# Optimization experiments

Hardware: AMD Instinct MI355X
Metric: run time of the kernel (lower is better)

The kernel has to match this reference:

```python
import jax, jax.numpy as jnp
import numpy as np

NUM_HEADS = 8
D_MODEL = 512
D_Q = D_MODEL // NUM_HEADS
B, S = 4, 2048


def setup_inputs() -> dict:
    key = jax.random.key(0)
    ks = jax.random.split(key, 7)
    bound = 1.0 / np.sqrt(D_MODEL)  # kaiming_uniform with a=sqrt(5) on fan_in=d_model
    return {
        "x_query": jax.random.normal(ks[0], (B, S, D_MODEL), dtype=jnp.float32),
        "x_key": jax.random.normal(ks[1], (B, S, D_MODEL), dtype=jnp.float32),
        "x_value": jax.random.normal(ks[2], (B, S, D_MODEL), dtype=jnp.float32),
        "Q": jax.random.uniform(ks[3], (NUM_HEADS, D_MODEL, D_Q), minval=-bound, maxval=bound, dtype=jnp.float32),
        "K": jax.random.uniform(ks[4], (NUM_HEADS, D_MODEL, D_Q), minval=-bound, maxval=bound, dtype=jnp.float32),
        "V": jax.random.uniform(ks[5], (NUM_HEADS, D_MODEL, D_Q), minval=-bound, maxval=bound, dtype=jnp.float32),
        "Wout": jax.random.uniform(ks[6], (D_MODEL, D_MODEL), minval=-bound, maxval=bound, dtype=jnp.float32),
    }


def reference(x_query, x_key, x_value, Q, K, V, Wout):
    # per-head projections: [B,S,d_model] x [H,d_model,d_q] -> [B,H,S,d_q]
    q = jnp.einsum('bsd,hdq->bhsq', x_query, Q)
    k = jnp.einsum('bsd,hdq->bhsq', x_key, K)
    v = jnp.einsum('bsd,hdq->bhsq', x_value, V)
    scale = 1.0 / jnp.sqrt(jnp.asarray(q.shape[-1], q.dtype))
    scores = jnp.einsum('bhsq,bhtq->bhst', q, k) * scale  # [B,H,S,S]
    attn = jax.nn.softmax(scores, axis=-1)
    heads = jnp.einsum('bhst,bhtq->bhsq', attn, v)  # [B,H,S,d_q]
    # faithful to original: .view(B, S, -1) on [B,H,S,d_q] layout (no transpose)
    concat = heads.reshape(heads.shape[0], heads.shape[2], -1)
    return concat @ Wout.T
```

## Files before the change

kernel.cpp:

```cpp
#include <hip/hip_runtime.h>
#include <math.h>

#define BATCH 4
#define SEQ   2048
#define DM    512
#define NH    8
#define DQ    64
#define BS    (BATCH*SEQ)
#define BPAD  72
#define APAD  72

#define QSCALE 0.18033688011112042f

typedef short  short8  __attribute__((ext_vector_type(8)));
typedef float  floatx4 __attribute__((ext_vector_type(4)));
typedef unsigned short ushort8 __attribute__((ext_vector_type(8)));

__device__ __forceinline__ unsigned short f2bf(float f) {
    return (unsigned short)((__float_as_uint(f) + 0x8000u) >> 16);
}
__device__ __forceinline__ unsigned pack2bf(float a, float b) {
    unsigned ua = __float_as_uint(a) + 0x8000u;
    unsigned ub = __float_as_uint(b) + 0x8000u;
    return __builtin_amdgcn_perm(ub, ua, 0x07060302u);
}

__global__ __launch_bounds__(256) void convert_w_kernel(
    const float* __restrict__ Wq, const float* __restrict__ Wk,
    const float* __restrict__ Wv, const float* __restrict__ Wo,
    unsigned short* __restrict__ wt, unsigned short* __restrict__ wo)
{
    const int which = blockIdx.y;
    const int idx = blockIdx.x * 256 + threadIdx.x;
    if (which == 3) {
        float4 v = *(const float4*)(Wo + (size_t)idx * 4);
        uint2 o;
        o.x = pack2bf(v.x, v.y);
        o.y = pack2bf(v.z, v.w);
        *(uint2*)(wo + (size_t)idx * 4) = o;
    } else {
        const float* W = (which == 0) ? Wq : (which == 1) ? Wk : Wv;
        const int n   = idx >> 7;
        const int dd0 = (idx & 127) * 4;
        const int h = n >> 6, d = n & 63;
        uint2 o;
        o.x = pack2bf(W[((size_t)h * DM + dd0 + 0) * DQ + d],
                      W[((size_t)h * DM + dd0 + 1) * DQ + d]);
        o.y = pack2bf(W[((size_t)h * DM + dd0 + 2) * DQ + d],
                      W[((size_t)h * DM + dd0 + 3) * DQ + d]);
        *(uint2*)(wt + (size_t)which * (DM * DM) + (size_t)n * DM + dd0) = o;
    }
}

__global__ __launch_bounds__(256) void qkv_gemm_kernel(
    const float* __restrict__ Xq, const float* __restrict__ Xk,
    const float* __restrict__ Xv, const unsigned short* __restrict__ wt,
    unsigned short* __restrict__ Oq, unsigned short* __restrict__ Ok,
    unsigned short* __restrict__ Ovt)
{
    __shared__ unsigned short As[128][APAD];
    __shared__ unsigned short Bs[128][APAD];

    const int which = blockIdx.z;
    const float* X = (which == 0) ? Xq : (which == 1) ? Xk : Xv;
    const unsigned short* Bt = wt + (size_t)which * (DM * DM);

    const int m0 = blockIdx.x * 128;
    const int n0 = blockIdx.y * 128;
    const int t = threadIdx.x, w = t >> 6, lane = t & 63;
    const int quad = lane >> 4, qr = lane & 15;
    const int arow = t >> 4;
    const int acol = (t & 15) * 4;
    const int brow = t >> 3;
    const int bcol = (t & 7) * 8;
    const int mw = 64 * (w >> 1), nw = 64 * (w & 1);

    floatx4 acc[4][4] = {};
    float4  areg[8];
    ushort8 breg[4];

    #pragma unroll
    for (int i = 0; i < 8; ++i)
        areg[i] = *(const float4*)(X + (size_t)(m0 + i * 16 + arow) * DM + acol);
    #pragma unroll
    for (int i = 0; i < 4; ++i)
        breg[i] = *(const ushort8*)(Bt + (size_t)(n0 + i * 32 + brow) * DM + bcol);

    for (int k0 = 0; k0 < DM; k0 += 64) {
        __syncthreads();
        #pragma unroll
        for (int i = 0; i < 8; ++i) {
            uint2 o;
            o.x = pack2bf(areg[i].x, areg[i].y);
            o.y = pack2bf(areg[i].z, areg[i].w);
            *(uint2*)&As[i * 16 + arow][acol] = o;
        }
        #pragma unroll
        for (int i = 0; i < 4; ++i)
            *(ushort8*)&Bs[i * 32 + brow][bcol] = breg[i];
        __syncthreads();

        if (k0 + 64 < DM) {
            #pragma unroll
            for (int i = 0; i < 8; ++i)
                areg[i] = *(const float4*)(X + (size_t)(m0 + i * 16 + arow) * DM + k0 + 64 + acol);
            #pragma unroll
            for (int i = 0; i < 4; ++i)
                breg[i] = *(const ushort8*)(Bt + (size_t)(n0 + i * 32 + brow) * DM + k0 + 64 + bcol);
        }

        #pragma unroll
        for (int kh = 0; kh < 2; ++kh) {
            short8 af[4], bf[4];
            #pragma unroll
            for (int si = 0; si < 4; ++si)
                af[si] = *(const short8*)&As[mw + 16 * si + qr][kh * 32 + quad * 8];
            #pragma unroll
            for (int sj = 0; sj < 4; ++sj)
                bf[sj] = *(const short8*)&Bs[nw + 16 * sj + qr][kh * 32 + quad * 8];
            #pragma unroll
            for (int si = 0; si < 4; ++si)
                #pragma unroll
                for (int sj = 0; sj < 4; ++sj)
                    acc[si][sj] = __builtin_amdgcn_mfma_f32_16x16x32_bf16(
                        af[si], bf[sj], acc[si][sj], 0, 0, 0);
        }
    }

    const float osc = (which == 0) ? QSCALE : 1.0f;
    if (which < 2) {
        unsigned short* O = (which == 0) ? Oq : Ok;
        #pragma unroll
        for (int si = 0; si < 4; ++si) {
            #pragma unroll
            for (int sj = 0; sj < 4; ++sj) {
                const int col = n0 + nw + 16 * sj + qr;
                const int h = col >> 6, d = col & 63;
                #pragma unroll
                for (int r = 0; r < 4; ++r) {
                    const int row = m0 + mw + 16 * si + quad * 4 + r;
                    const int b = row >> 11, s = row & (SEQ - 1);
                    O[((size_t)(b * NH + h) * SEQ + s) * DQ + d] = f2bf(acc[si][sj][r] * osc);
                }
            }
        }
    } else {
        #pragma unroll
        for (int si = 0; si < 4; ++si) {
            #pragma unroll
            for (int sj = 0; sj < 4; ++sj) {
                const int col = n0 + nw + 16 * sj + qr;
                const int h = col >> 6, d = col & 63;
                #pragma unroll
                for (int r = 0; r < 4; ++r) {
                    const int row = m0 + mw + 16 * si + quad * 4 + r;
                    const int b = row >> 11, s = row & (SEQ - 1);
                    Ovt[((size_t)(b * NH + h) * DQ + d) * SEQ + s] = f2bf(acc[si][sj][r]);
                }
            }
        }
    }
}

__global__ __launch_bounds__(256) void out_gemm_kernel(
    const unsigned short* __restrict__ A, const unsigned short* __restrict__ Bt,
    float* __restrict__ C)
{
    __shared__ unsigned short As[64][APAD];
    __shared__ unsigned short Bs[128][APAD];

    const int m0 = blockIdx.x * 64;
    const int n0 = blockIdx.y * 128;
    const int t = threadIdx.x, w = t >> 6, lane = t & 63;
    const int quad = lane >> 4, qr = lane & 15;
    const int brow = t >> 3;
    const int bcol = (t & 7) * 8;
    const int mw = 32 * (w >> 1), nw = 64 * (w & 1);

    floatx4 acc[2][4] = {};
    ushort8 areg[2], breg[4];

    #pragma unroll
    for (int i = 0; i < 2; ++i)
        areg[i] = *(const ushort8*)(A + (size_t)(m0 + i * 32 + brow) * DM + bcol);
    #pragma unroll
    for (int i = 0; i < 4; ++i)
        breg[i] = *(const ushort8*)(Bt + (size_t)(n0 + i * 32 + brow) * DM + bcol);

    for (int k0 = 0; k0 < DM; k0 += 64) {
        __syncthreads();
        #pragma unroll
        for (int i = 0; i < 2; ++i)
            *(ushort8*)&As[i * 32 + brow][bcol] = areg[i];
        #pragma unroll
        for (int i = 0; i < 4; ++i)
            *(ushort8*)&Bs[i * 32 + brow][bcol] = breg[i];
        __syncthreads();

        if (k0 + 64 < DM) {
            #pragma unroll
            for (int i = 0; i < 2; ++i)
                areg[i] = *(const ushort8*)(A + (size_t)(m0 + i * 32 + brow) * DM + k0 + 64 + bcol);
            #pragma unroll
            for (int i = 0; i < 4; ++i)
                breg[i] = *(const ushort8*)(Bt + (size_t)(n0 + i * 32 + brow) * DM + k0 + 64 + bcol);
        }

        #pragma unroll
        for (int kh = 0; kh < 2; ++kh) {
            short8 af[2], bf[4];
            #pragma unroll
            for (int si = 0; si < 2; ++si)
                af[si] = *(const short8*)&As[mw + 16 * si + qr][kh * 32 + quad * 8];
            #pragma unroll
            for (int sj = 0; sj < 4; ++sj)
                bf[sj] = *(const short8*)&Bs[nw + 16 * sj + qr][kh * 32 + quad * 8];
            #pragma unroll
            for (int si = 0; si < 2; ++si)
                #pragma unroll
                for (int sj = 0; sj < 4; ++sj)
                    acc[si][sj] = __builtin_amdgcn_mfma_f32_16x16x32_bf16(
                        af[si], bf[sj], acc[si][sj], 0, 0, 0);
        }
    }

    #pragma unroll
    for (int si = 0; si < 2; ++si) {
        #pragma unroll
        for (int sj = 0; sj < 4; ++sj) {
            const int col = n0 + nw + 16 * sj + qr;
            #pragma unroll
            for (int r = 0; r < 4; ++r) {
                const int row = m0 + mw + 16 * si + quad * 4 + r;
                C[(size_t)row * DM + col] = acc[si][sj][r];
            }
        }
    }
}

__global__ __launch_bounds__(256) void attn_kernel(
    const unsigned short* __restrict__ Qp, const unsigned short* __restrict__ Kp,
    const unsigned short* __restrict__ Vtp, unsigned short* __restrict__ Hd)
{
    __shared__ unsigned short Qs[64][BPAD];
    __shared__ unsigned short Ks[64][BPAD];
    __shared__ unsigned short Vts[64][BPAD];
    __shared__ unsigned short Ps[64][BPAD];

    const int s0 = blockIdx.x * 64;
    const int h  = blockIdx.y;
    const int b  = blockIdx.z;
    const size_t bh    = (size_t)(b * NH + h);
    const size_t base  = bh * SEQ * DQ;
    const size_t vbase = bh * DQ * SEQ;

    const int t    = threadIdx.x;
    const int w    = t >> 6;
    const int lane = t & 63;
    const int quad = lane >> 4;
    const int qr   = lane & 15;

    {
        const unsigned short* g = Qp + base + (size_t)s0 * DQ;
        #pragma unroll
        for (int i = 0; i < 2; ++i) {
            const int c = t + 256 * i;
            const int row = c >> 3, col8 = (c & 7) * 8;
            *(ushort8*)&Qs[row][col8] = *(const ushort8*)(g + row * DQ + col8);
        }
    }
    __syncthreads();
    const short8 aq0 = *(const short8*)&Qs[16 * w + qr][quad * 8];
    const short8 aq1 = *(const short8*)&Qs[16 * w + qr][quad * 8 + 32];

    floatx4 acc_o[4] = {};
    float l_lane = 0.f;

    ushort8 kreg[2], vreg[2];
    {
        const unsigned short* gk = Kp + base;
        const unsigned short* gv = Vtp + vbase;
        #pragma unroll
        for (int i = 0; i < 2; ++i) {
            const int c = t + 256 * i;
            const int row = c >> 3, col8 = (c & 7) * 8;
            kreg[i] = *(const ushort8*)(gk + row * DQ + col8);
            vreg[i] = *(const ushort8*)(gv + (size_t)row * SEQ + col8);
        }
    }

    for (int kt = 0; kt < SEQ; kt += 64) {
        __syncthreads();
        #pragma unroll
        for (int i = 0; i < 2; ++i) {
            const int c = t + 256 * i;
            const int row = c >> 3, col8 = (c & 7) * 8;
            *(ushort8*)&Ks[row][col8]  = kreg[i];
            *(ushort8*)&Vts[row][col8] = vreg[i];
        }
        __syncthreads();

        if (kt + 64 < SEQ) {
            const unsigned short* gk = Kp + base + (size_t)(kt + 64) * DQ;
            const unsigned short* gv = Vtp + vbase + (kt + 64);
            #pragma unroll
            for (int i = 0; i < 2; ++i) {
                const int c = t + 256 * i;
                const int row = c >> 3, col8 = (c & 7) * 8;
                kreg[i] = *(const ushort8*)(gk + row * DQ + col8);
                vreg[i] = *(const ushort8*)(gv + (size_t)row * SEQ + col8);
            }
        }

        #pragma unroll
        for (int si = 0; si < 4; ++si) {
            const short8 ak0 = *(const short8*)&Ks[16 * si + qr][quad * 8];
            const short8 ak1 = *(const short8*)&Ks[16 * si + qr][quad * 8 + 32];
            floatx4 z = {0.f, 0.f, 0.f, 0.f};
            z = __builtin_amdgcn_mfma_f32_16x16x32_bf16(ak0, aq0, z, 0, 0, 0);
            z = __builtin_amdgcn_mfma_f32_16x16x32_bf16(ak1, aq1, z, 0, 0, 0);
            const float p0 = __builtin_amdgcn_exp2f(z[0]);
            const float p1 = __builtin_amdgcn_exp2f(z[1]);
            const float p2 = __builtin_amdgcn_exp2f(z[2]);
            const float p3 = __builtin_amdgcn_exp2f(z[3]);
            l_lane += (p0 + p1) + (p2 + p3);
            uint2 pk;
            pk.x = pack2bf(p0, p1);
            pk.y = pack2bf(p2, p3);
            *(uint2*)&Ps[16 * w + qr][16 * si + quad * 4] = pk;
        }

        const short8 ap0 = *(const short8*)&Ps[16 * w + qr][quad * 8];
        const short8 ap1 = *(const short8*)&Ps[16 * w + qr][quad * 8 + 32];
        #pragma unroll
        for (int c = 0; c < 4; ++c) {
            const short8 bv0 = *(const short8*)&Vts[16 * c + qr][quad * 8];
            const short8 bv1 = *(const short8*)&Vts[16 * c + qr][quad * 8 + 32];
            acc_o[c] = __builtin_amdgcn_mfma_f32_16x16x32_bf16(ap0, bv0, acc_o[c], 0, 0, 0);
            acc_o[c] = __builtin_amdgcn_mfma_f32_16x16x32_bf16(ap1, bv1, acc_o[c], 0, 0, 0);
        }
    }

    l_lane += __shfl_xor(l_lane, 16);
    l_lane += __shfl_xor(l_lane, 32);
    float inv_l[4];
    #pragma unroll
    for (int r = 0; r < 4; ++r)
        inv_l[r] = 1.0f / __shfl(l_lane, quad * 4 + r);

    #pragma unroll
    for (int c = 0; c < 4; ++c)
        #pragma unroll
        for (int r = 0; r < 4; ++r)
            Hd[base + (size_t)(s0 + 16 * w + quad * 4 + r) * DQ + 16 * c + qr] =
                f2bf(acc_o[c][r] * inv_l[r]);
}

extern "C" void kernel_launch(void* const* d_in, const int* in_sizes, int n_in,
                              void* d_out, int out_size, void* d_ws, size_t ws_size,
                              hipStream_t stream) {
    const float* xq = (const float*)d_in[0];
    const float* xk = (const float*)d_in[1];
    const float* xv = (const float*)d_in[2];
    const float* Qw = (const float*)d_in[3];
    const float* Kw = (const float*)d_in[4];
    const float* Vw = (const float*)d_in[5];
    const float* Wo = (const float*)d_in[6];
    float* out = (float*)d_out;

    unsigned short* ws = (unsigned short*)d_ws;
    unsigned short* wt    = ws;
    unsigned short* wo    = ws + (size_t)786432;
    unsigned short* q_ws  = ws + (size_t)1048576;
    unsigned short* k_ws  = ws + (size_t)5242880;
    unsigned short* vt_ws = ws + (size_t)9437184;
    unsigned short* h_ws  = ws + (size_t)13631488;

    convert_w_kernel<<<dim3(256, 4), 256, 0, stream>>>(Qw, Kw, Vw, Wo, wt, wo);
    qkv_gemm_kernel<<<dim3(64, 4, 3), 256, 0, stream>>>(xq, xk, xv, wt, q_ws, k_ws, vt_ws);
    attn_kernel<<<dim3(SEQ / 64, NH, BATCH), 256, 0, stream>>>(q_ws, k_ws, vt_ws, h_ws);
    out_gemm_kernel<<<dim3(128, 4), 256, 0, stream>>>(h_ws, wo, out);
}
```

Measured before the change: 197.0 us.

## Switch attention to 32x32x16 MFMA with a 2x2 wave split and cross-wave reduction

```diff
diff --git a/kernel.cpp b/kernel.cpp
--- a/kernel.cpp
+++ b/kernel.cpp
@@ -12,8 +12,9 @@
 
 #define QSCALE 0.18033688011112042f
 
-typedef short  short8  __attribute__((ext_vector_type(8)));
-typedef float  floatx4 __attribute__((ext_vector_type(4)));
+typedef short  short8   __attribute__((ext_vector_type(8)));
+typedef float  floatx4  __attribute__((ext_vector_type(4)));
+typedef float  floatx16 __attribute__((ext_vector_type(16)));
 typedef unsigned short ushort8 __attribute__((ext_vector_type(8)));
 
 __device__ __forceinline__ unsigned short f2bf(float f) {
@@ -238,14 +239,15 @@
     }
 }
 
-__global__ __launch_bounds__(256) void attn_kernel(
+__global__ __launch_bounds__(256, 4) void attn_kernel(
     const unsigned short* __restrict__ Qp, const unsigned short* __restrict__ Kp,
     const unsigned short* __restrict__ Vtp, unsigned short* __restrict__ Hd)
 {
-    __shared__ unsigned short Qs[64][BPAD];
-    __shared__ unsigned short Ks[64][BPAD];
-    __shared__ unsigned short Vts[64][BPAD];
-    __shared__ unsigned short Ps[64][BPAD];
+    __shared__ unsigned short smem[4 * 64 * BPAD];
+    unsigned short (*Qs)[BPAD]  = (unsigned short (*)[BPAD])(smem);
+    unsigned short (*Ks)[BPAD]  = (unsigned short (*)[BPAD])(smem + 64 * BPAD);
+    unsigned short (*Vts)[BPAD] = (unsigned short (*)[BPAD])(smem + 2 * 64 * BPAD);
+    unsigned short (*Ps)[BPAD]  = (unsigned short (*)[BPAD])(smem + 3 * 64 * BPAD);
 
     const int s0 = blockIdx.x * 64;
     const int h  = blockIdx.y;
@@ -257,8 +259,10 @@
     const int t    = threadIdx.x;
     const int w    = t >> 6;
     const int lane = t & 63;
-    const int quad = lane >> 4;
-    const int qr   = lane & 15;
+    const int qh   = w >> 1;
+    const int kh   = w & 1;
+    const int ln31 = lane & 31;
+    const int lh   = lane >> 5;
 
     {
         const unsigned short* g = Qp + base + (size_t)s0 * DQ;
@@ -270,10 +274,12 @@
         }
     }
     __syncthreads();
-    const short8 aq0 = *(const short8*)&Qs[16 * w + qr][quad * 8];
-    const short8 aq1 = *(const short8*)&Qs[16 * w + qr][quad * 8 + 32];
-
-    floatx4 acc_o[4] = {};
+    short8 bq[4];
+    #pragma unroll
+    for (int s = 0; s < 4; ++s)
+        bq[s] = *(const short8*)&Qs[32 * qh + ln31][16 * s + lh * 8];
+
+    floatx16 accO[2] = {};
     float l_lane = 0.f;
 
     ushort8 kreg[2], vreg[2];
@@ -312,48 +318,69 @@
             }
         }
 
-        #pragma unroll
-        for (int si = 0; si < 4; ++si) {
-            const short8 ak0 = *(const short8*)&Ks[16 * si + qr][quad * 8];
-            const short8 ak1 = *(const short8*)&Ks[16 * si + qr][quad * 8 + 32];
-            floatx4 z = {0.f, 0.f, 0.f, 0.f};
-            z = __builtin_amdgcn_mfma_f32_16x16x32_bf16(ak0, aq0, z, 0, 0, 0);
-            z = __builtin_amdgcn_mfma_f32_16x16x32_bf16(ak1, aq1, z, 0, 0, 0);
-            const float p0 = __builtin_amdgcn_exp2f(z[0]);
-            const float p1 = __builtin_amdgcn_exp2f(z[1]);
-            const float p2 = __builtin_amdgcn_exp2f(z[2]);
-            const float p3 = __builtin_amdgcn_exp2f(z[3]);
+        floatx16 z = {};
+        #pragma unroll
+        for (int s = 0; s < 4; ++s) {
+            const short8 ak = *(const short8*)&Ks[32 * kh + ln31][16 * s + lh * 8];
+            z = __builtin_amdgcn_mfma_f32_32x32x16_bf16(ak, bq[s], z, 0, 0, 0);
+        }
+
+        #pragma unroll
+        for (int g = 0; g < 4; ++g) {
+            const float p0 = __builtin_amdgcn_exp2f(z[4 * g + 0]);
+            const float p1 = __builtin_amdgcn_exp2f(z[4 * g + 1]);
+            const float p2 = __builtin_amdgcn_exp2f(z[4 * g + 2]);
+            const float p3 = __builtin_amdgcn_exp2f(z[4 * g + 3]);
             l_lane += (p0 + p1) + (p2 + p3);
             uint2 pk;
             pk.x = pack2bf(p0, p1);
             pk.y = pack2bf(p2, p3);
-            *(uint2*)&Ps[16 * w + qr][16 * si + quad * 4] = pk;
-        }
-
-        const short8 ap0 = *(const short8*)&Ps[16 * w + qr][quad * 8];
-        const short8 ap1 = *(const short8*)&Ps[16 * w + qr][quad * 8 + 32];
-        #pragma unroll
-        for (int c = 0; c < 4; ++c) {
-            const short8 bv0 = *(const short8*)&Vts[16 * c + qr][quad * 8];
-            const short8 bv1 = *(const short8*)&Vts[16 * c + qr][quad * 8 + 32];
-            acc_o[c] = __builtin_amdgcn_mfma_f32_16x16x32_bf16(ap0, bv0, acc_o[c], 0, 0, 0);
-            acc_o[c] = __builtin_amdgcn_mfma_f32_16x16x32_bf16(ap1, bv1, acc_o[c], 0, 0, 0);
-        }
-    }
-
-    l_lane += __shfl_xor(l_lane, 16);
-    l_lane += __shfl_xor(l_lane, 32);
-    float inv_l[4];
-    #pragma unroll
-    for (int r = 0; r < 4; ++r)
-        inv_l[r] = 1.0f / __shfl(l_lane, quad * 4 + r);
-
-    #pragma unroll
-    for (int c = 0; c < 4; ++c)
-        #pragma unroll
-        for (int r = 0; r < 4; ++r)
-            Hd[base + (size_t)(s0 + 16 * w + quad * 4 + r) * DQ + 16 * c + qr] =
-                f2bf(acc_o[c][r] * inv_l[r]);
+            *(uint2*)&Ps[32 * qh + ln31][32 * kh + 8 * g + 4 * lh] = pk;
+        }
+
+        short8 ap[2];
+        ap[0] = *(const short8*)&Ps[32 * qh + ln31][32 * kh + lh * 8];
+        ap[1] = *(const short8*)&Ps[32 * qh + ln31][32 * kh + 16 + lh * 8];
+        #pragma unroll
+        for (int a = 0; a < 2; ++a) {
+            #pragma unroll
+            for (int s = 0; s < 2; ++s) {
+                const short8 bv = *(const short8*)&Vts[32 * a + ln31][32 * kh + 16 * s + lh * 8];
+                accO[a] = __builtin_amdgcn_mfma_f32_32x32x16_bf16(ap[s], bv, accO[a], 0, 0, 0);
+            }
+        }
+    }
+
+    float l2 = l_lane + __shfl_xor(l_lane, 32);
+    float* Obuf = (float*)(smem + 64 * BPAD);
+    float* lbuf = (float*)(smem + 3 * 64 * BPAD);
+    __syncthreads();
+
+    if (kh == 0) {
+        if (lane < 32) lbuf[qh * 32 + lane] = l2;
+        #pragma unroll
+        for (int a = 0; a < 2; ++a)
+            #pragma unroll
+            for (int r = 0; r < 16; ++r) {
+                const int qrow = (r & 3) + 8 * (r >> 2) + 4 * lh;
+                Obuf[(32 * qh + qrow) * 66 + 32 * a + ln31] = accO[a][r];
+            }
+    }
+    __syncthreads();
+
+    if (kh == 1) {
+        const float ltot = l2 + lbuf[qh * 32 + ln31];
+        if (lane < 32) lbuf[64 + qh * 32 + lane] = 1.0f / ltot;
+        #pragma unroll
+        for (int a = 0; a < 2; ++a)
+            #pragma unroll
+            for (int r = 0; r < 16; ++r) {
+                const int qrow = (r & 3) + 8 * (r >> 2) + 4 * lh;
+                const float o = accO[a][r] + Obuf[(32 * qh + qrow) * 66 + 32 * a + ln31];
+                const float iv = lbuf[64 + qh * 32 + qrow];
+                Hd[base + (size_t)(s0 + 32 * qh + qrow) * DQ + 32 * a + ln31] = f2bf(o * iv);
+            }
+    }
 }
 
 extern "C" void kernel_launch(void* const* d_in, const int* in_sizes, int n_in,
```

Measured after the change: 186.8 us. 5.2% less time.
